# Optimization experiments

Hardware: AMD Instinct MI355X
Metric: run time of the kernel (lower is better)

Reference implementation:

```python
import jax, jax.numpy as jnp
import numpy as np
import math

ACCBLOCK = 32
SPLITS = 2


def _mam(x, w, accblock):
    """MAM fully-connected: block-accumulate products along K, then max+min over blocks.
    x: [M, K], w: [K, N]  ->  [M, N] = max_blk(partial) + min_blk(partial)
    Implemented as a scan over blocks with running max/min to avoid a [M, nblk, N] tensor.
    """
    M, K = x.shape
    N = w.shape[1]
    nblk = K // accblock
    assert nblk * accblock == K
    xb = x.reshape(M, nblk, accblock).transpose(1, 0, 2)  # [nblk, M, B]
    wb = w.reshape(nblk, accblock, N)                      # [nblk, B, N]
    big = jnp.asarray(jnp.finfo(x.dtype).max, x.dtype)

    def step(carry, blk):
        mx, mn = carry
        xi, wi = blk                      # [M, B], [B, N]
        s = xi @ wi                       # block partial sum [M, N]
        return (jnp.maximum(mx, s), jnp.minimum(mn, s)), None

    init = (jnp.full((M, N), -big, x.dtype), jnp.full((M, N), big, x.dtype))
    (mx, mn), _ = jax.lax.scan(step, init, (xb, wb))
    return mx + mn


def reference(x, weight, bias):
    # eval mode, vcon_steps=0 -> alpha=1, beta=0; no weight dropout, no output dropout
    in_features = weight.shape[1]
    w = weight.T  # [K, N]
    sub = math.ceil(in_features / SPLITS)
    last = in_features - sub * (SPLITS - 1)
    out = _mam(x[:, :sub], w[:sub], ACCBLOCK)
    for i in range(1, SPLITS - 1):
        out = out + _mam(x[:, i * sub:(i + 1) * sub], w[i * sub:(i + 1) * sub], ACCBLOCK)
    out = out + _mam(x[:, in_features - last:], w[in_features - last:], ACCBLOCK)
    return out + bias[None, :]


def setup_inputs() -> dict:
    key = jax.random.key(0)
    k1, k2, k3 = jax.random.split(key, 3)
    M, K, N = 2048, 4096, 4096
    x = jax.random.normal(k1, (M, K), dtype=jnp.float32)
    weight = jax.random.normal(k2, (N, K), dtype=jnp.float32) * (1.0 / math.sqrt(K))
    bias = jax.random.normal(k3, (N,), dtype=jnp.float32) * (1.0 / math.sqrt(K))
    return {"x": x, "weight": weight, "bias": bias}
```

## Files before the change

### kernel.cpp

```cpp
#include <hip/hip_runtime.h>
#include <cstdint>
#include <cstddef>

typedef __bf16 bf16;
typedef __bf16 bf16x4 __attribute__((ext_vector_type(4)));
typedef __bf16 bf16x8 __attribute__((ext_vector_type(8)));
typedef float  f32x4  __attribute__((ext_vector_type(4)));

#define MDIM 2048
#define NDIM 4096
#define KDIM 4096
#define FLOATMAX 3.402823466e38f

__global__ void cvt2_f32_to_bf16(const float* __restrict__ x, const float* __restrict__ w,
                                 bf16* __restrict__ xb, bf16* __restrict__ wb,
                                 int xn4, int wn4) {
    const int stride = gridDim.x * blockDim.x;
    int i = blockIdx.x * blockDim.x + threadIdx.x;
    for (int k = i; k < xn4; k += stride) {
        f32x4 v = reinterpret_cast<const f32x4*>(x)[k];
        reinterpret_cast<bf16x4*>(xb)[k] = __builtin_convertvector(v, bf16x4);
    }
    for (int k = i; k < wn4; k += stride) {
        f32x4 v = reinterpret_cast<const f32x4*>(w)[k];
        reinterpret_cast<bf16x4*>(wb)[k] = __builtin_convertvector(v, bf16x4);
    }
}

__device__ __forceinline__ void g2lds16(const bf16* g, bf16* l) {
    __builtin_amdgcn_global_load_lds(
        (const __attribute__((address_space(1))) uint32_t*)g,
        (__attribute__((address_space(3))) uint32_t*)l, 16, 0, 0);
}

__global__ __launch_bounds__(512, 2) void mam_kernel(
    const bf16* __restrict__ A,
    const bf16* __restrict__ B,
    const float* __restrict__ bias,
    float* __restrict__ out)
{
    __shared__ __align__(16) bf16 sA[2][2][128 * 32];
    __shared__ __align__(16) bf16 sB[2][2][128 * 32];

    const int t    = threadIdx.x;
    const int lane = t & 63;
    const int w    = t >> 6;
    const int wm   = (w >> 2) * 64;
    const int wn   = (w & 3) * 32;

    const int m0 = blockIdx.y * 128;
    const int n0 = blockIdx.x * 128;

    const int srow   = t >> 2;
    const int spos   = t & 3;
    const int schunk = spos ^ ((srow >> 1) & 3);
    const bf16* gA = A + (size_t)(m0 + srow) * KDIM + schunk * 8;
    const bf16* gB = B + (size_t)(n0 + srow) * KDIM + schunk * 8;
    const int ldst = t * 8;

    const int frow = lane & 15;
    const int q    = lane >> 4;
    int offA[4], offB[2];
#pragma unroll
    for (int i = 0; i < 4; ++i) {
        const int R = wm + i * 16 + frow;
        offA[i] = R * 32 + (q ^ ((R >> 1) & 3)) * 8;
    }
#pragma unroll
    for (int j = 0; j < 2; ++j) {
        const int R = wn + j * 16 + frow;
        offB[j] = R * 32 + (q ^ ((R >> 1) & 3)) * 8;
    }

    const f32x4 kZero = {0.f, 0.f, 0.f, 0.f};

    f32x4 acc[4][2], mx[4][2], mn[4][2];
#pragma unroll
    for (int i = 0; i < 4; ++i)
#pragma unroll
        for (int j = 0; j < 2; ++j) {
            acc[i][j] = kZero;
            mx[i][j] = (f32x4)(-FLOATMAX);
            mn[i][j] = (f32x4)(FLOATMAX);
        }

    auto prefetch = [&](int s, int pb) {
        const bf16* ga = gA + (size_t)s * 64;
        const bf16* gb = gB + (size_t)s * 64;
        g2lds16(ga,      &sA[pb][0][ldst]);
        g2lds16(ga + 32, &sA[pb][1][ldst]);
        g2lds16(gb,      &sB[pb][0][ldst]);
        g2lds16(gb + 32, &sB[pb][1][ldst]);
    };

    auto compute = [&](int pb) {
        bf16x8 aF0[4], aF1[4], bF0[2], bF1[2];
#pragma unroll
        for (int i = 0; i < 4; ++i) {
            aF0[i] = *(const bf16x8*)&sA[pb][0][offA[i]];
            aF1[i] = *(const bf16x8*)&sA[pb][1][offA[i]];
        }
#pragma unroll
        for (int j = 0; j < 2; ++j) {
            bF0[j] = *(const bf16x8*)&sB[pb][0][offB[j]];
            bF1[j] = *(const bf16x8*)&sB[pb][1][offB[j]];
        }
#pragma unroll
        for (int i = 0; i < 4; ++i) {
#pragma unroll
            for (int j = 0; j < 2; ++j) {
                f32x4 s0 = __builtin_amdgcn_mfma_f32_16x16x32_bf16(
                    aF0[i], bF0[j], kZero, 0, 0, 0);
                f32x4 s1 = __builtin_amdgcn_mfma_f32_16x16x32_bf16(
                    aF1[i], bF1[j], kZero, 0, 0, 0);
#pragma unroll
                for (int r = 0; r < 4; ++r) {
                    mx[i][j][r] = fmaxf(fmaxf(mx[i][j][r], s0[r]), s1[r]);
                    mn[i][j][r] = fminf(fminf(mn[i][j][r], s0[r]), s1[r]);
                }
            }
        }
    };

    auto split_reset = [&]() {
#pragma unroll
        for (int i = 0; i < 4; ++i)
#pragma unroll
            for (int j = 0; j < 2; ++j) {
                acc[i][j] += mx[i][j] + mn[i][j];
                mx[i][j] = (f32x4)(-FLOATMAX);
                mn[i][j] = (f32x4)(FLOATMAX);
            }
    };

    prefetch(0, 0);

    int bb = 0;
#pragma unroll 1
    for (int it = 0; it < 32; ++it) {
        __syncthreads();
        prefetch(bb + 1, 1);
        compute(0);
        ++bb;
        __syncthreads();
        if (bb < 63) prefetch(bb + 1, 0);
        compute(1);
        if (bb == 31 || bb == 63) split_reset();
        ++bb;
    }

    const int orow = (lane >> 4) * 4;
    const int ocol = lane & 15;
#pragma unroll
    for (int j = 0; j < 2; ++j) {
        const int col = n0 + wn + j * 16 + ocol;
        const float bv = bias[col];
#pragma unroll
        for (int i = 0; i < 4; ++i) {
            const int row = m0 + wm + i * 16 + orow;
#pragma unroll
            for (int r = 0; r < 4; ++r) {
                out[(size_t)(row + r) * NDIM + col] = acc[i][j][r] + bv;
            }
        }
    }
}

extern "C" void kernel_launch(void* const* d_in, const int* in_sizes, int n_in,
                              void* d_out, int out_size, void* d_ws, size_t ws_size,
                              hipStream_t stream) {
    const float* x    = (const float*)d_in[0];
    const float* wgt  = (const float*)d_in[1];
    const float* bias = (const float*)d_in[2];
    float* out = (float*)d_out;

    bf16* xbf = (bf16*)d_ws;
    bf16* wbf = xbf + (size_t)MDIM * KDIM;

    const int xn4 = (MDIM * KDIM) / 4;
    const int wn4 = (NDIM * KDIM) / 4;
    cvt2_f32_to_bf16<<<dim3(4096), dim3(256), 0, stream>>>(x, wgt, xbf, wbf, xn4, wn4);

    dim3 grid(NDIM / 128, MDIM / 128);
    mam_kernel<<<grid, dim3(512), 0, stream>>>(xbf, wbf, bias, out);
}
```

Before: 251.8 us.

## Halve block to 4 waves with 64x64 warp tiles and spill split partial to output

The block shrinks from 8 to 4 wavefronts, each now computing a 64x64 sub-tile, so every LDS fragment load feeds more MFMAs. Each thread issues twice as many global-to-LDS copies. To make room for the larger mx/mn register set, the running accumulator is dropped. The first split's result is written straight to the output buffer, then read back and added at the end. This raises register pressure per wave and adds an extra global read/write pass over the output, in exchange for better fragment reuse and fewer waves contending for LDS.

```diff
diff --git a/kernel.cpp b/kernel.cpp
--- a/kernel.cpp
+++ b/kernel.cpp
@@ -33,7 +33,7 @@
         (__attribute__((address_space(3))) uint32_t*)l, 16, 0, 0);
 }
 
-__global__ __launch_bounds__(512, 2) void mam_kernel(
+__global__ __launch_bounds__(256, 2) void mam_kernel(
     const bf16* __restrict__ A,
     const bf16* __restrict__ B,
     const float* __restrict__ bias,
@@ -45,8 +45,8 @@
     const int t    = threadIdx.x;
     const int lane = t & 63;
     const int w    = t >> 6;
-    const int wm   = (w >> 2) * 64;
-    const int wn   = (w & 3) * 32;
+    const int wm   = (w >> 1) * 64;
+    const int wn   = (w & 1) * 64;
 
     const int m0 = blockIdx.y * 128;
     const int n0 = blockIdx.x * 128;
@@ -60,26 +60,22 @@
 
     const int frow = lane & 15;
     const int q    = lane >> 4;
-    int offA[4], offB[2];
+    int offA[4], offB[4];
 #pragma unroll
     for (int i = 0; i < 4; ++i) {
-        const int R = wm + i * 16 + frow;
-        offA[i] = R * 32 + (q ^ ((R >> 1) & 3)) * 8;
-    }
-#pragma unroll
-    for (int j = 0; j < 2; ++j) {
-        const int R = wn + j * 16 + frow;
-        offB[j] = R * 32 + (q ^ ((R >> 1) & 3)) * 8;
+        const int Ra = wm + i * 16 + frow;
+        offA[i] = Ra * 32 + (q ^ ((Ra >> 1) & 3)) * 8;
+        const int Rb = wn + i * 16 + frow;
+        offB[i] = Rb * 32 + (q ^ ((Rb >> 1) & 3)) * 8;
     }
 
     const f32x4 kZero = {0.f, 0.f, 0.f, 0.f};
 
-    f32x4 acc[4][2], mx[4][2], mn[4][2];
+    f32x4 mx[4][4], mn[4][4];
 #pragma unroll
     for (int i = 0; i < 4; ++i)
 #pragma unroll
-        for (int j = 0; j < 2; ++j) {
-            acc[i][j] = kZero;
+        for (int j = 0; j < 4; ++j) {
             mx[i][j] = (f32x4)(-FLOATMAX);
             mn[i][j] = (f32x4)(FLOATMAX);
         }
@@ -87,28 +83,29 @@
     auto prefetch = [&](int s, int pb) {
         const bf16* ga = gA + (size_t)s * 64;
         const bf16* gb = gB + (size_t)s * 64;
-        g2lds16(ga,      &sA[pb][0][ldst]);
-        g2lds16(ga + 32, &sA[pb][1][ldst]);
-        g2lds16(gb,      &sB[pb][0][ldst]);
-        g2lds16(gb + 32, &sB[pb][1][ldst]);
+        g2lds16(ga,                  &sA[pb][0][ldst]);
+        g2lds16(ga + 64 * KDIM,      &sA[pb][0][2048 + ldst]);
+        g2lds16(ga + 32,             &sA[pb][1][ldst]);
+        g2lds16(ga + 64 * KDIM + 32, &sA[pb][1][2048 + ldst]);
+        g2lds16(gb,                  &sB[pb][0][ldst]);
+        g2lds16(gb + 64 * KDIM,      &sB[pb][0][2048 + ldst]);
+        g2lds16(gb + 32,             &sB[pb][1][ldst]);
+        g2lds16(gb + 64 * KDIM + 32, &sB[pb][1][2048 + ldst]);
     };
 
     auto compute = [&](int pb) {
-        bf16x8 aF0[4], aF1[4], bF0[2], bF1[2];
+        bf16x8 aF0[4], aF1[4], bF0[4], bF1[4];
 #pragma unroll
         for (int i = 0; i < 4; ++i) {
             aF0[i] = *(const bf16x8*)&sA[pb][0][offA[i]];
             aF1[i] = *(const bf16x8*)&sA[pb][1][offA[i]];
-        }
-#pragma unroll
-        for (int j = 0; j < 2; ++j) {
-            bF0[j] = *(const bf16x8*)&sB[pb][0][offB[j]];
-            bF1[j] = *(const bf16x8*)&sB[pb][1][offB[j]];
+            bF0[i] = *(const bf16x8*)&sB[pb][0][offB[i]];
+            bF1[i] = *(const bf16x8*)&sB[pb][1][offB[i]];
         }
 #pragma unroll
         for (int i = 0; i < 4; ++i) {
 #pragma unroll
-            for (int j = 0; j < 2; ++j) {
+            for (int j = 0; j < 4; ++j) {
                 f32x4 s0 = __builtin_amdgcn_mfma_f32_16x16x32_bf16(
                     aF0[i], bF0[j], kZero, 0, 0, 0);
                 f32x4 s1 = __builtin_amdgcn_mfma_f32_16x16x32_bf16(
@@ -122,15 +119,23 @@
         }
     };
 
-    auto split_reset = [&]() {
+    const int orow = (lane >> 4) * 4;
+    const int ocol = lane & 15;
+
+    auto split_store_reset = [&]() {
 #pragma unroll
-        for (int i = 0; i < 4; ++i)
+        for (int j = 0; j < 4; ++j) {
+            const int col = n0 + wn + j * 16 + ocol;
 #pragma unroll
-            for (int j = 0; j < 2; ++j) {
-                acc[i][j] += mx[i][j] + mn[i][j];
+            for (int i = 0; i < 4; ++i) {
+                const int row = m0 + wm + i * 16 + orow;
+#pragma unroll
+                for (int r = 0; r < 4; ++r)
+                    out[(size_t)(row + r) * NDIM + col] = mx[i][j][r] + mn[i][j][r];
                 mx[i][j] = (f32x4)(-FLOATMAX);
                 mn[i][j] = (f32x4)(FLOATMAX);
             }
+        }
     };
 
     prefetch(0, 0);
@@ -145,14 +150,12 @@
         __syncthreads();
         if (bb < 63) prefetch(bb + 1, 0);
         compute(1);
-        if (bb == 31 || bb == 63) split_reset();
+        if (bb == 31) split_store_reset();
         ++bb;
     }
 
-    const int orow = (lane >> 4) * 4;
-    const int ocol = lane & 15;
 #pragma unroll
-    for (int j = 0; j < 2; ++j) {
+    for (int j = 0; j < 4; ++j) {
         const int col = n0 + wn + j * 16 + ocol;
         const float bv = bias[col];
 #pragma unroll
@@ -160,7 +163,8 @@
             const int row = m0 + wm + i * 16 + orow;
 #pragma unroll
             for (int r = 0; r < 4; ++r) {
-                out[(size_t)(row + r) * NDIM + col] = acc[i][j][r] + bv;
+                const size_t idx = (size_t)(row + r) * NDIM + col;
+                out[idx] = out[idx] + (mx[i][j][r] + mn[i][j][r]) + bv;
             }
         }
     }
@@ -182,5 +186,5 @@
     cvt2_f32_to_bf16<<<dim3(4096), dim3(256), 0, stream>>>(x, wgt, xbf, wbf, xn4, wn4);
 
     dim3 grid(NDIM / 128, MDIM / 128);
-    mam_kernel<<<grid, dim3(512), 0, stream>>>(xbf, wbf, bias, out);
+    mam_kernel<<<grid, dim3(256), 0, stream>>>(xbf, wbf, bias, out);
 }
```

New measurement: 481.3 us. 1.91x slower.

## Deepen LDS pipeline to four stages with explicit vmcnt waits

Applied to the files above, without the earlier changes.

Replaces the double-buffered LDS scheme with a four-buffer ring that keeps three global-to-LDS loads in flight, using explicit s_waitcnt vmcnt counts and raw s_barrier instead of __syncthreads. Fragment offsets are simplified to a single base plus constant strides, which works because the swizzle depends only on frow. This is meant to hide global load latency better. LDS use doubles to 64KB per block, which could cut occupancy at two blocks per CU. The hand-counted vmcnt waits are correct only if the compiler emits exactly four loads per stage.

```diff
diff --git a/kernel.cpp b/kernel.cpp
--- a/kernel.cpp
+++ b/kernel.cpp
@@ -33,14 +33,16 @@
         (__attribute__((address_space(3))) uint32_t*)l, 16, 0, 0);
 }
 
+#define WAITVM(N) asm volatile("s_waitcnt vmcnt(" #N ")" ::: "memory")
+
 __global__ __launch_bounds__(512, 2) void mam_kernel(
     const bf16* __restrict__ A,
     const bf16* __restrict__ B,
     const float* __restrict__ bias,
     float* __restrict__ out)
 {
-    __shared__ __align__(16) bf16 sA[2][2][128 * 32];
-    __shared__ __align__(16) bf16 sB[2][2][128 * 32];
+    __shared__ __align__(16) bf16 sA[4][2][128 * 32];
+    __shared__ __align__(16) bf16 sB[4][2][128 * 32];
 
     const int t    = threadIdx.x;
     const int lane = t & 63;
@@ -60,17 +62,9 @@
 
     const int frow = lane & 15;
     const int q    = lane >> 4;
-    int offA[4], offB[2];
-#pragma unroll
-    for (int i = 0; i < 4; ++i) {
-        const int R = wm + i * 16 + frow;
-        offA[i] = R * 32 + (q ^ ((R >> 1) & 3)) * 8;
-    }
-#pragma unroll
-    for (int j = 0; j < 2; ++j) {
-        const int R = wn + j * 16 + frow;
-        offB[j] = R * 32 + (q ^ ((R >> 1) & 3)) * 8;
-    }
+    const int swz  = (q ^ ((frow >> 1) & 3)) * 8;
+    const int offA0 = (wm + frow) * 32 + swz;
+    const int offB0 = (wn + frow) * 32 + swz;
 
     const f32x4 kZero = {0.f, 0.f, 0.f, 0.f};
 
@@ -84,26 +78,27 @@
             mn[i][j] = (f32x4)(FLOATMAX);
         }
 
-    auto prefetch = [&](int s, int pb) {
+    auto prefetch = [&](int s) {
+        const int buf = s & 3;
         const bf16* ga = gA + (size_t)s * 64;
         const bf16* gb = gB + (size_t)s * 64;
-        g2lds16(ga,      &sA[pb][0][ldst]);
-        g2lds16(ga + 32, &sA[pb][1][ldst]);
-        g2lds16(gb,      &sB[pb][0][ldst]);
-        g2lds16(gb + 32, &sB[pb][1][ldst]);
+        g2lds16(ga,      &sA[buf][0][ldst]);
+        g2lds16(ga + 32, &sA[buf][1][ldst]);
+        g2lds16(gb,      &sB[buf][0][ldst]);
+        g2lds16(gb + 32, &sB[buf][1][ldst]);
     };
 
-    auto compute = [&](int pb) {
+    auto compute = [&](int buf) {
         bf16x8 aF0[4], aF1[4], bF0[2], bF1[2];
 #pragma unroll
-        for (int i = 0; i < 4; ++i) {
-            aF0[i] = *(const bf16x8*)&sA[pb][0][offA[i]];
-            aF1[i] = *(const bf16x8*)&sA[pb][1][offA[i]];
+        for (int j = 0; j < 2; ++j) {
+            bF0[j] = *(const bf16x8*)&sB[buf][0][offB0 + j * 512];
+            bF1[j] = *(const bf16x8*)&sB[buf][1][offB0 + j * 512];
         }
 #pragma unroll
-        for (int j = 0; j < 2; ++j) {
-            bF0[j] = *(const bf16x8*)&sB[pb][0][offB[j]];
-            bF1[j] = *(const bf16x8*)&sB[pb][1][offB[j]];
+        for (int i = 0; i < 4; ++i) {
+            aF0[i] = *(const bf16x8*)&sA[buf][0][offA0 + i * 512];
+            aF1[i] = *(const bf16x8*)&sA[buf][1][offA0 + i * 512];
         }
 #pragma unroll
         for (int i = 0; i < 4; ++i) {
@@ -133,20 +128,25 @@
             }
     };
 
-    prefetch(0, 0);
+    prefetch(0);
+    prefetch(1);
+    prefetch(2);
+    WAITVM(8);
+    __builtin_amdgcn_s_barrier();
+    __builtin_amdgcn_sched_barrier(0);
 
-    int bb = 0;
 #pragma unroll 1
-    for (int it = 0; it < 32; ++it) {
-        __syncthreads();
-        prefetch(bb + 1, 1);
-        compute(0);
-        ++bb;
-        __syncthreads();
-        if (bb < 63) prefetch(bb + 1, 0);
-        compute(1);
-        if (bb == 31 || bb == 63) split_reset();
-        ++bb;
+    for (int s = 0; s < 64; ++s) {
+        if (s < 61) prefetch(s + 3);
+        compute(s & 3);
+        if (s == 31 || s == 63) split_reset();
+        if (s < 63) {
+            if (s < 61)       { WAITVM(8); }
+            else if (s == 61) { WAITVM(4); }
+            else              { WAITVM(0); }
+            __builtin_amdgcn_s_barrier();
+            __builtin_amdgcn_sched_barrier(0);
+        }
     }
 
     const int orow = (lane >> 4) * 4;
```

Measured after the change: 281.9 us. +11.9%, slower.
